# Kernel tuning notes

Hardware: AMD Instinct MI355X
Metric: run time of the kernel (lower is better)

## Reference

```python
import jax, jax.numpy as jnp
import numpy as np

SIGMA = 1.0   # noise std (unit-variance synthetic input)
P = 11        # patch size p1
K = 16        # number of similar patches k1
WIN = 65      # search window w (odd)
S = 3         # reference-patch stride
ALPHA = 0.5   # n2n alpha


def _unfold(x, ksize, stride):
    # (N,1,H,W) -> (N, ksize*ksize, Ho, Wo); kernel positions row-major (== torch F.unfold for C=1)
    return jax.lax.conv_general_dilated_patches(
        x, (ksize, ksize), (stride, stride), 'VALID',
        dimension_numbers=('NCHW', 'OIHW', 'NCHW'))


def block_matching(x, k, p, w, s):
    N, _, H, W = x.shape
    v = w // 2
    assert (H - p + 1) % s == 1 and (W - p + 1) % s == 1  # no edge-case branches needed
    Href = (H - p) // s + 1
    Wref = (W - p) // s + 1
    x_pad = jnp.pad(x, ((0, 0), (0, 0), (v, v), (v, v)))  # zero pad; invalid candidates masked below
    # |patch|^2 / p^2 at every position of the padded image (== F.avg_pool2d(x**2, p))
    sq = jax.lax.reduce_window(x_pad * x_pad, 0.0, jax.lax.add,
                               (1, 1, p, p), (1, 1, 1, 1), 'VALID') / (p * p)
    norms = _unfold(sq, 2 * v + 1, s)                                  # (N,(2v+1)^2,Href,Wref)
    norms = norms.reshape(N, 2 * v + 1, 2 * v + 1, Href, Wref).transpose(0, 3, 4, 1, 2)
    lw = _unfold(x_pad, 2 * v + p, s) / p                              # (N,(2v+p)^2,Href,Wref)
    lw = lw.reshape(N, 2 * v + p, 2 * v + p, Href, Wref).transpose(0, 3, 4, 1, 2)
    G = N * Href * Wref
    lw = lw.reshape(1, G, 2 * v + p, 2 * v + p)
    ref = lw[0, :, v:-v, v:-v][:, None]                                # (G,1,p,p) reference patches
    sp = jax.lax.conv_general_dilated(
        lw, ref, (1, 1), 'VALID',
        dimension_numbers=('NCHW', 'OIHW', 'NCHW'),
        feature_group_count=G)                                         # (1,G,2v+1,2v+1)
    dist = norms.reshape(1, G, 2 * v + 1, 2 * v + 1) - 2.0 * sp
    dist = dist.reshape(N, Href, Wref, 2 * v + 1, 2 * v + 1)
    # mask candidate patches that fall outside the original image (torch uses NaN padding + topk)
    offs = jnp.arange(-v, v + 1)
    hr = jnp.arange(Href) * s
    wr = jnp.arange(Wref) * s
    row_ok = (hr[:, None] + offs >= 0) & (hr[:, None] + offs <= H - p)  # (Href, 2v+1)
    col_ok = (wr[:, None] + offs >= 0) & (wr[:, None] + offs <= W - p)  # (Wref, 2v+1)
    valid = row_ok[:, None, :, None] & col_ok[None, :, None, :]
    dist = jnp.where(valid[None], dist, jnp.inf)
    dist = dist.at[..., v, v].set(-jnp.inf)                            # reference patch always kept
    dist = dist.reshape(N, Href, Wref, (2 * v + 1) ** 2)
    _, idx = jax.lax.top_k(-dist, k)                                   # k smallest distances
    ind_row = idx // (2 * v + 1) - v
    ind_col = idx % (2 * v + 1) - v
    ind = (ind_row + hr[None, :, None, None]) * (W - p + 1) + (ind_col + wr[None, None, :, None])
    return ind.reshape(N, -1)                                          # (N, Href*Wref*k)


def gather_groups(y, indices, k, p):
    N = y.shape[0]
    uf = _unfold(y, p, 1).reshape(N, p * p, -1)                        # (N, n, (H-p+1)(W-p+1))
    Yg = jnp.take_along_axis(uf, indices[:, None, :], axis=2)          # (N, n, L*k)
    L = indices.shape[1] // k
    return Yg.reshape(N, p * p, L, k).transpose(0, 2, 3, 1)            # (N, L, k, n)


def denoise1(Y, sigma):
    # method='n2n', constraints='affine'
    N, B, k, n = Y.shape
    D = n * sigma ** 2
    E = n * ALPHA ** 2 * sigma ** 2
    Ik = jnp.eye(k, dtype=Y.dtype)
    Q = Y @ jnp.swapaxes(Y, 2, 3) + E * Ik                             # (N,B,k,k), SPD
    Lc = jnp.linalg.cholesky(Q)
    Ikb = jnp.broadcast_to(Ik, Q.shape)
    Z = jax.scipy.linalg.solve_triangular(Lc, Ikb, lower=True)
    Qinv = jax.scipy.linalg.solve_triangular(jnp.swapaxes(Lc, 2, 3), Z, lower=False)
    Qinv1 = jnp.sum(Qinv, axis=3, keepdims=True)
    Qinv2 = jnp.sum(Qinv1, axis=2, keepdims=True)
    theta = Ik - (Qinv - (Qinv1 @ jnp.swapaxes(Qinv1, 2, 3)) / Qinv2) * (D + E)
    theta = jnp.swapaxes(theta, 2, 3)
    X_hat = theta @ Y
    weights = 1.0 / jnp.clip(jnp.sum(theta * theta, axis=3, keepdims=True), 1.0 / k, 1.0)
    return X_hat, weights


def _fold(x, H, W, p):
    # inverse of unfold: sum overlapping p x p patches back onto the image grid
    N, n, _ = x.shape
    Hp, Wp = H - p + 1, W - p + 1
    x = x.reshape(N, p, p, Hp, Wp)
    out = jnp.zeros((N, 1, H, W), x.dtype)
    for a in range(p):
        for b in range(p):
            out = out.at[:, 0, a:a + Hp, b:b + Wp].add(x[:, a, b])
    return out


def aggregate(X_hat, weights, indices, H, W, p):
    N, L, k, n = X_hat.shape
    X = (X_hat * weights).reshape(N, L * k, n).transpose(0, 2, 1)      # (N, n, L*k)
    Wt = jnp.broadcast_to(weights, (N, L, k, n)).reshape(N, L * k, n).transpose(0, 2, 1)
    Lfull = (H - p + 1) * (W - p + 1)
    def scat(vals, idx):
        return jnp.zeros((n, Lfull), vals.dtype).at[:, idx].add(vals)
    X_sum = jax.vmap(scat)(X, indices)
    W_sum = jax.vmap(scat)(Wt, indices)
    return _fold(X_sum, H, W, p) / _fold(W_sum, H, W, p)


def _forward(y):
    N, C, H, W = y.shape
    indices = block_matching(y, K, P, WIN, S)
    Yg = gather_groups(y, indices, K, P)
    X_hat, weights = denoise1(Yg, SIGMA)
    return aggregate(X_hat, weights, indices, H, W, P)


def setup_inputs():
    key = jax.random.key(0)
    y = jax.random.normal(key, (4, 1, 128, 128), dtype=jnp.float32)
    return {"y": y}


def reference(y):
    return _forward(y)
```

## Files before the change

### kernel.cpp

```cpp
#include <hip/hip_runtime.h>
#include <math.h>

#define HH 128
#define WW 128
#define NIMG 4
#define PP 11
#define KSIM 16
#define STRIDE_S 3
#define VRAD 32
#define WINW 65
#define NTASK (WINW*9)
#define HREF 40
#define WREF 40
#define NPOS 118
#define WROWS 75
#define WPITCH 84
#define NGROUP (NIMG*HREF*WREF)
#define EPS_E 30.25f
#define DE_C 151.25f
#define INFD 3.0e38f
#define RTASK (VRAD*9 + VRAD/8)

#define TDIM 4
#define NTIL (HREF/TDIM)
#define FOOT 84
#define FPITCH 85

__global__ __launch_bounds__(256, 4)
void bm_kernel(const float* __restrict__ y, int* __restrict__ inds)
{
    __shared__ float win[WROWS][WPITCH];
    __shared__ float swv[4];
    __shared__ int   swi[4];

    const int blk = blockIdx.x;
    const int n   = blk / (HREF*WREF);
    const int rem = blk % (HREF*WREF);
    const int hr  = (rem / WREF) * STRIDE_S;
    const int wr  = (rem % WREF) * STRIDE_S;
    const float* img = y + n * HH * WW;
    const int tid = threadIdx.x;

    for (int t = tid; t < WROWS * WPITCH; t += 256) {
        int r = t / WPITCH, c = t % WPITCH;
        int gr = hr - VRAD + r, gc = wr - VRAD + c;
        float v = 0.f;
        if (c < WROWS && gr >= 0 && gr < HH && gc >= 0 && gc < WW)
            v = img[gr * WW + gc];
        win[r][c] = v;
    }
    __syncthreads();

    float d[3][8];
#pragma unroll
    for (int s = 0; s < 3; s++)
#pragma unroll
        for (int c = 0; c < 8; c++) d[s][c] = INFD;

#pragma unroll
    for (int s = 0; s < 3; s++) {
        int task = tid + (s << 8);
        if (task < NTASK) {
            int drx = task / 9;
            int c0  = (task % 9) * 8;
            int rr  = hr + drx - VRAD;
            bool rowok = (rr >= 0 && rr <= HH - PP);
            if (rowok) {
                float dot[8];
                float colsq[18];
#pragma unroll
                for (int c = 0; c < 8; c++) dot[c] = 0.f;
#pragma unroll
                for (int j2 = 0; j2 < 18; j2++) colsq[j2] = 0.f;
                for (int a = 0; a < PP; a++) {
                    const float* wrow = &win[drx + a][c0];
                    const float* rrow = &win[VRAD + a][VRAD];
                    float wv[18];
#pragma unroll
                    for (int j2 = 0; j2 < 18; j2++) wv[j2] = wrow[j2];
#pragma unroll
                    for (int j2 = 0; j2 < 18; j2++) colsq[j2] += wv[j2] * wv[j2];
#pragma unroll
                    for (int b = 0; b < PP; b++) {
                        float rv = rrow[b];
#pragma unroll
                        for (int c = 0; c < 8; c++)
                            dot[c] += wv[b + c] * rv;
                    }
                }
#pragma unroll
                for (int j2 = 1; j2 < 18; j2++) colsq[j2] += colsq[j2 - 1];
#pragma unroll
                for (int c = 0; c < 8; c++) {
                    int dcx = c0 + c;
                    int cc  = wr + dcx - VRAD;
                    float norm = colsq[c + 10] - (c ? colsq[c - 1] : 0.f);
                    if (dcx < WINW && cc >= 0 && cc <= WW - PP)
                        d[s][c] = norm - 2.f * dot[c];
                }
            }
            if (task == RTASK) d[s][0] = -INFD;
        }
    }

    float lval = INFD; int lidx = 0;
#pragma unroll
    for (int s = 0; s < 3; s++)
#pragma unroll
        for (int c = 0; c < 8; c++)
            if (d[s][c] < lval) { lval = d[s][c]; lidx = (s << 3) | c; }

    for (int sel = 0; sel < KSIM; sel++) {
        float rv = lval;
        int   ri = ((tid + ((lidx >> 3) << 8)) << 3) | (lidx & 7);
#pragma unroll
        for (int off = 32; off > 0; off >>= 1) {
            float ov = __shfl_down(rv, off);
            int   oi = __shfl_down(ri, off);
            if (ov < rv) { rv = ov; ri = oi; }
        }
        if ((tid & 63) == 0) { swv[tid >> 6] = rv; swi[tid >> 6] = ri; }
        __syncthreads();
        float bval = swv[0]; int bidx = swi[0];
#pragma unroll
        for (int w2 = 1; w2 < 4; w2++)
            if (swv[w2] < bval) { bval = swv[w2]; bidx = swi[w2]; }
        if (tid == 0) {
            int task = bidx >> 3;
            int drx = task / 9, dcx = (task % 9) * 8 + (bidx & 7);
            int prr = hr + drx - VRAD, pcc = wr + dcx - VRAD;
            inds[blk * KSIM + sel] = prr * NPOS + pcc;
        }
        __syncthreads();
        int otid = (bidx >> 3) & 255;
        if (tid == otid) {
            int code = (((bidx >> 3) >> 8) << 3) | (bidx & 7);
            lval = INFD; lidx = 0;
#pragma unroll
            for (int s = 0; s < 3; s++)
#pragma unroll
                for (int c = 0; c < 8; c++) {
                    if (((s << 3) | c) == code) d[s][c] = INFD;
                    if (d[s][c] < lval) { lval = d[s][c]; lidx = (s << 3) | c; }
                }
        }
    }
}

__global__ __launch_bounds__(256, 2)
void dn_kernel(const float* __restrict__ y, const int* __restrict__ inds,
               float2* __restrict__ nd, int R)
{
    __shared__ float2 acc[FOOT][FPITCH];

    const int blk = blockIdx.x;
    const int n  = blk / (NTIL*NTIL);
    const int tr = blk % (NTIL*NTIL);
    const int ti = tr / NTIL, tj = tr % NTIL;
    const int tid = threadIdx.x;
    const int r0 = 3*(ti*TDIM) - VRAD;
    const int c0 = 3*(tj*TDIM) - VRAD;
    const float* img = y + n * HH * WW;

    {
        float* af = (float*)acc;
        for (int t = tid; t < FOOT*FPITCH*2; t += 256) af[t] = 0.f;
    }
    __syncthreads();

    const int wv2  = tid >> 6;
    const int lane = tid & 63;
    const int sg   = lane >> 4;
    const int r    = lane & 15;
    const int g    = n * (HREF*WREF) + (ti*TDIM + wv2) * WREF + (tj*TDIM + sg);

    const int idx  = inds[g * KSIM + r];
    const int prow = idx / NPOS, pcol = idx % NPOS;
    const float* pbase = img + prow * WW + pcol;

    float q[16];
#pragma unroll
    for (int m = 0; m < 16; m++) q[m] = (m == r) ? EPS_E : 0.f;
    for (int a = 0; a < PP; a++) {
        float yr[PP];
#pragma unroll
        for (int b = 0; b < PP; b++) yr[b] = pbase[a * WW + b];
#pragma unroll
        for (int b = 0; b < PP; b++) {
            float yj = yr[b];
#pragma unroll
            for (int m = 0; m < 16; m++) {
                float ym = __shfl(yj, m, 16);
                q[m] += yj * ym;
            }
        }
    }

#pragma unroll
    for (int c = 0; c < 16; c++) {
        float dc = __shfl(q[c], c, 16);
        float s  = sqrtf(dc);
        float inv = 1.f / s;
        q[c] = (r == c) ? s : q[c] * inv;
#pragma unroll
        for (int b = c + 1; b < 16; b++) {
            float lb = __shfl(q[c], b, 16);
            q[b] -= q[c] * lb;
        }
    }

    float z[16];
#pragma unroll
    for (int rr = 0; rr < 16; rr++) {
        float s = (rr == r) ? 1.f : 0.f;
        float diag = 0.f;
#pragma unroll
        for (int m = 0; m <= rr; m++) {
            float lrm = __shfl(q[m], rr, 16);
            if (m < rr) s -= lrm * z[m];
            else diag = lrm;
        }
        z[rr] = s / diag;
    }
    float x[16];
#pragma unroll
    for (int rr = 15; rr >= 0; rr--) {
        float s = z[rr];
        float diag = 0.f;
#pragma unroll
        for (int m = 15; m >= rr; m--) {
            float lmr = __shfl(q[rr], m, 16);
            if (m > rr) s -= lmr * x[m];
            else diag = lmr;
        }
        x[rr] = s / diag;
    }

    float s1 = 0.f;
#pragma unroll
    for (int b = 0; b < 16; b++) s1 += x[b];
    float s2 = s1;
#pragma unroll
    for (int mask = 1; mask < 16; mask <<= 1) s2 += __shfl_xor(s2, mask, 16);
    float th[16], tsq = 0.f;
#pragma unroll
    for (int b = 0; b < 16; b++) {
        float s1b = __shfl(s1, b, 16);
        float t = ((b == r) ? 1.f : 0.f) - (x[b] - s1 * s1b / s2) * DE_C;
        th[b] = t;
        tsq += t * t;
    }
    tsq = fminf(fmaxf(tsq, 1.f / (float)KSIM), 1.f);
    const float w = 1.f / tsq;

    const int arow = prow - r0, acol = pcol - c0;
    for (int a = 0; a < PP; a++) {
        float yr[PP];
#pragma unroll
        for (int b = 0; b < PP; b++) yr[b] = pbase[a * WW + b];
#pragma unroll
        for (int b = 0; b < PP; b++) {
            float yj = yr[b];
            float xh = 0.f;
#pragma unroll
            for (int m = 0; m < 16; m++) {
                float ym = __shfl(yj, m, 16);
                xh += th[m] * ym;
            }
            float2* cell = &acc[arow + a][acol + b];
            atomicAdd(&cell->x, w * xh);
            atomicAdd(&cell->y, w);
        }
    }
    __syncthreads();

    float2* ndI = nd + ((size_t)(blk & (R - 1)) * NIMG + n) * HH * WW;
    for (int t = tid; t < FOOT * FOOT; t += 256) {
        int rr = t / FOOT, cc = t % FOOT;
        float2 v = acc[rr][cc];
        if (v.y != 0.f) {
            int gr = r0 + rr, gc = c0 + cc;
            int px = gr * WW + gc;
#if defined(__has_builtin) && __has_builtin(__builtin_amdgcn_global_atomic_fadd_v2f32)
            typedef float v2f __attribute__((ext_vector_type(2)));
            __builtin_amdgcn_global_atomic_fadd_v2f32((v2f*)&ndI[px], (v2f){v.x, v.y});
#else
            atomicAdd(&ndI[px].x, v.x);
            atomicAdd(&ndI[px].y, v.y);
#endif
        }
    }
}

__global__ __launch_bounds__(256)
void fin_kernel(const float2* __restrict__ nd, float* __restrict__ out, int R)
{
    int t = blockIdx.x * 256 + threadIdx.x;
    if (t < NIMG * HH * WW) {
        float sn = 0.f, sd = 0.f;
        for (int r = 0; r < R; r++) {
            float2 v = nd[(size_t)r * NIMG * HH * WW + t];
            sn += v.x; sd += v.y;
        }
        out[t] = sn / sd;
    }
}

extern "C" void kernel_launch(void* const* d_in, const int* in_sizes, int n_in,
                              void* d_out, int out_size, void* d_ws, size_t ws_size,
                              hipStream_t stream)
{
    const float* y = (const float*)d_in[0];
    float* out = (float*)d_out;

    size_t indsBytes = (size_t)NGROUP * KSIM * sizeof(int);
    size_t perRep    = (size_t)NIMG * HH * WW * sizeof(float2);
    int R = 1;
    while (R < 4 && indsBytes + perRep * (size_t)(R * 2) <= ws_size) R <<= 1;

    float2* nd  = (float2*)d_ws;
    int*    inds = (int*)((char*)d_ws + perRep * (size_t)R);

    hipMemsetAsync(nd, 0, perRep * (size_t)R, stream);
    bm_kernel<<<NGROUP, 256, 0, stream>>>(y, inds);
    dn_kernel<<<NIMG * NTIL * NTIL, 256, 0, stream>>>(y, inds, nd, R);
    fin_kernel<<<(NIMG * HH * WW + 255) / 256, 256, 0, stream>>>(nd, out, R);
}
```

Measured before the change: 476.6 us.

## Rewrite denoise kernel with shared-memory tile and Gauss-Jordan inverse, vectorize BM loads

The denoise kernel now stages the image footprint in shared memory, computes the 16 Gram matrices cooperatively across 512 threads, and inverts them with a parallel Gauss-Jordan sweep in LDS. This replaces the per-lane shuffle-based Cholesky and triangular solves. The output projection is then done as a small matmul with shared atomics. The block-matching kernel switches to float4/float2 LDS loads and raises its occupancy hint. In exchange, Gauss-Jordan without pivoting needs more barriers and may be less numerically stable than Cholesky.

```diff
diff --git a/kernel.cpp b/kernel.cpp
--- a/kernel.cpp
+++ b/kernel.cpp
@@ -21,12 +21,11 @@
 #define INFD 3.0e38f
 #define RTASK (VRAD*9 + VRAD/8)
 
-#define TDIM 4
-#define NTIL (HREF/TDIM)
 #define FOOT 84
 #define FPITCH 85
-
-__global__ __launch_bounds__(256, 4)
+#define SPITCH 88
+
+__global__ __launch_bounds__(256, 5)
 void bm_kernel(const float* __restrict__ y, int* __restrict__ inds)
 {
     __shared__ float win[WROWS][WPITCH];
@@ -73,19 +72,25 @@
 #pragma unroll
                 for (int j2 = 0; j2 < 18; j2++) colsq[j2] = 0.f;
                 for (int a = 0; a < PP; a++) {
-                    const float* wrow = &win[drx + a][c0];
-                    const float* rrow = &win[VRAD + a][VRAD];
-                    float wv[18];
-#pragma unroll
-                    for (int j2 = 0; j2 < 18; j2++) wv[j2] = wrow[j2];
+                    const float4* w4 = reinterpret_cast<const float4*>(&win[drx + a][c0]);
+                    float4 A0 = w4[0], A1 = w4[1], A2 = w4[2], A3 = w4[3];
+                    float2 A4 = *reinterpret_cast<const float2*>(&win[drx + a][c0 + 16]);
+                    float wv[18] = {A0.x,A0.y,A0.z,A0.w, A1.x,A1.y,A1.z,A1.w,
+                                    A2.x,A2.y,A2.z,A2.w, A3.x,A3.y,A3.z,A3.w,
+                                    A4.x,A4.y};
+                    const float4* r4 = reinterpret_cast<const float4*>(&win[VRAD + a][VRAD]);
+                    float4 R0 = r4[0], R1 = r4[1];
+                    float2 R2 = *reinterpret_cast<const float2*>(&win[VRAD + a][VRAD + 8]);
+                    float  R3 = win[VRAD + a][VRAD + 10];
+                    float rv[11] = {R0.x,R0.y,R0.z,R0.w, R1.x,R1.y,R1.z,R1.w,
+                                    R2.x,R2.y, R3};
 #pragma unroll
                     for (int j2 = 0; j2 < 18; j2++) colsq[j2] += wv[j2] * wv[j2];
 #pragma unroll
                     for (int b = 0; b < PP; b++) {
-                        float rv = rrow[b];
 #pragma unroll
                         for (int c = 0; c < 8; c++)
-                            dot[c] += wv[b + c] * rv;
+                            dot[c] += wv[b + c] * rv[b];
                     }
                 }
 #pragma unroll
@@ -147,140 +152,176 @@
     }
 }
 
-__global__ __launch_bounds__(256, 2)
+__global__ __launch_bounds__(512, 1)
 void dn_kernel(const float* __restrict__ y, const int* __restrict__ inds,
                float2* __restrict__ nd, int R)
 {
+    __shared__ float  src[FOOT][SPITCH];
     __shared__ float2 acc[FOOT][FPITCH];
+    __shared__ float  Qm[16][16][17];
+    __shared__ float  s1[16][16];
+    __shared__ float  s2[16];
+    __shared__ float  wl[16][16];
+    __shared__ short  pr_[16][16], pc_[16][16];
 
     const int blk = blockIdx.x;
-    const int n  = blk / (NTIL*NTIL);
-    const int tr = blk % (NTIL*NTIL);
-    const int ti = tr / NTIL, tj = tr % NTIL;
+    const int n  = blk / 100;
+    const int tr = blk % 100;
+    const int ti = tr / 10, tj = tr % 10;
+    const int r0 = 12*ti - VRAD, c0 = 12*tj - VRAD;
     const int tid = threadIdx.x;
-    const int r0 = 3*(ti*TDIM) - VRAD;
-    const int c0 = 3*(tj*TDIM) - VRAD;
     const float* img = y + n * HH * WW;
 
+    if (tid < 256) {
+        int g = tid >> 4, m = tid & 15;
+        int gg = n*(HREF*WREF) + (ti*4 + (g >> 2))*WREF + (tj*4 + (g & 3));
+        int idx = inds[gg*KSIM + m];
+        pr_[g][m] = (short)(idx / NPOS);
+        pc_[g][m] = (short)(idx % NPOS);
+    }
+    for (int t = tid; t < FOOT*FOOT; t += 512) {
+        int rr = t / FOOT, cc = t % FOOT;
+        int gr = r0 + rr, gc = c0 + cc;
+        float v = 0.f;
+        if (gr >= 0 && gr < HH && gc >= 0 && gc < WW) v = img[gr*WW + gc];
+        src[rr][cc] = v;
+    }
+    for (int t = tid; t < FOOT*FPITCH; t += 512)
+        acc[t/FPITCH][t%FPITCH] = make_float2(0.f, 0.f);
+    __syncthreads();
+
+    for (int k = 0; k < 5; k++) {
+        int task = tid + k*512;
+        if (task < 16*136) {
+            int g = task / 136, e = task % 136;
+            int i = (int)((sqrtf(8.f*(float)e + 1.f) - 1.f) * 0.5f + 1e-4f);
+            int j = e - i*(i+1)/2;
+            int ari = pr_[g][i] - r0, aci = pc_[g][i] - c0;
+            int arj = pr_[g][j] - r0, acj = pc_[g][j] - c0;
+            float s = (i == j) ? EPS_E : 0.f;
+            for (int a = 0; a < PP; a++) {
+                const float* Ri = &src[ari + a][aci];
+                const float* Rj = &src[arj + a][acj];
+#pragma unroll
+                for (int b = 0; b < PP; b++) s += Ri[b] * Rj[b];
+            }
+            Qm[g][i][j] = s;
+            Qm[g][j][i] = s;
+        }
+    }
+    __syncthreads();
+
+    const int uu = tid >> 8, ii = (tid >> 4) & 15, jj = tid & 15;
+    for (int ks = 0; ks < 16; ks++) {
+        float fA[8], rk[8], pv[8], aij[8];
+#pragma unroll
+        for (int k = 0; k < 8; k++) {
+            int g = uu + 2*k;
+            fA[k]  = Qm[g][ii][ks];
+            rk[k]  = Qm[g][ks][jj];
+            pv[k]  = Qm[g][ks][ks];
+            aij[k] = Qm[g][ii][jj];
+        }
+        __syncthreads();
+#pragma unroll
+        for (int k = 0; k < 8; k++) {
+            int g = uu + 2*k;
+            float inv = 1.f / pv[k];
+            float nv;
+            if (ii == ks) nv = (jj == ks) ? inv : rk[k] * inv;
+            else          nv = (jj == ks) ? -fA[k] * inv : aij[k] - fA[k] * rk[k] * inv;
+            Qm[g][ii][jj] = nv;
+        }
+        __syncthreads();
+    }
+
+    if (tid < 256) {
+        int g = tid >> 4, a = tid & 15;
+        float s = 0.f;
+#pragma unroll
+        for (int b = 0; b < 16; b++) s += Qm[g][a][b];
+        s1[g][a] = s;
+    }
+    __syncthreads();
+    if (tid < 16) {
+        float s = 0.f;
+#pragma unroll
+        for (int a = 0; a < 16; a++) s += s1[tid][a];
+        s2[tid] = s;
+    }
+    __syncthreads();
+#pragma unroll
+    for (int k = 0; k < 8; k++) {
+        int g = uu + 2*k;
+        float t = ((ii == jj) ? 1.f : 0.f)
+                - (Qm[g][ii][jj] - s1[g][ii]*s1[g][jj]/s2[g]) * DE_C;
+        Qm[g][ii][jj] = t;
+    }
+    __syncthreads();
+    if (tid < 256) {
+        int g = tid >> 4, r = tid & 15;
+        float s = 0.f;
+#pragma unroll
+        for (int m2 = 0; m2 < 16; m2++) { float t = Qm[g][m2][r]; s += t*t; }
+        s = fminf(fmaxf(s, 1.f/16.f), 1.f);
+        wl[g][r] = 1.f / s;
+    }
+    __syncthreads();
+
     {
-        float* af = (float*)acc;
-        for (int t = tid; t < FOOT*FPITCH*2; t += 256) af[t] = 0.f;
-    }
-    __syncthreads();
-
-    const int wv2  = tid >> 6;
-    const int lane = tid & 63;
-    const int sg   = lane >> 4;
-    const int r    = lane & 15;
-    const int g    = n * (HREF*WREF) + (ti*TDIM + wv2) * WREF + (tj*TDIM + sg);
-
-    const int idx  = inds[g * KSIM + r];
-    const int prow = idx / NPOS, pcol = idx % NPOS;
-    const float* pbase = img + prow * WW + pcol;
-
-    float q[16];
-#pragma unroll
-    for (int m = 0; m < 16; m++) q[m] = (m == r) ? EPS_E : 0.f;
-    for (int a = 0; a < PP; a++) {
-        float yr[PP];
-#pragma unroll
-        for (int b = 0; b < PP; b++) yr[b] = pbase[a * WW + b];
-#pragma unroll
-        for (int b = 0; b < PP; b++) {
-            float yj = yr[b];
-#pragma unroll
-            for (int m = 0; m < 16; m++) {
-                float ym = __shfl(yj, m, 16);
-                q[m] += yj * ym;
+        const int g6 = tid >> 5, q6 = tid & 31;
+        const int pxb = q6 * 4;
+        int drp[4], dcp[4]; bool okp[4];
+#pragma unroll
+        for (int p = 0; p < 4; p++) {
+            int px = pxb + p;
+            okp[p] = (px < 121);
+            int pxc = okp[p] ? px : 0;
+            drp[p] = pxc / 11; dcp[p] = pxc % 11;
+        }
+        float xh[16][4];
+#pragma unroll
+        for (int r = 0; r < 16; r++)
+#pragma unroll
+            for (int p = 0; p < 4; p++) xh[r][p] = 0.f;
+#pragma unroll
+        for (int m2 = 0; m2 < 16; m2++) {
+            int ar = pr_[g6][m2] - r0, ac = pc_[g6][m2] - c0;
+            float tv[16];
+#pragma unroll
+            for (int r = 0; r < 16; r++) tv[r] = Qm[g6][m2][r];
+            float yv[4];
+#pragma unroll
+            for (int p = 0; p < 4; p++) yv[p] = src[ar + drp[p]][ac + dcp[p]];
+#pragma unroll
+            for (int r = 0; r < 16; r++)
+#pragma unroll
+                for (int p = 0; p < 4; p++) xh[r][p] += tv[r] * yv[p];
+        }
+#pragma unroll
+        for (int r = 0; r < 16; r++) {
+            int ar = pr_[g6][r] - r0, ac = pc_[g6][r] - c0;
+            float wv2 = wl[g6][r];
+#pragma unroll
+            for (int p = 0; p < 4; p++) {
+                if (okp[p]) {
+                    float* cell = (float*)&acc[ar + drp[p]][ac + dcp[p]];
+                    __hip_atomic_fetch_add(cell,     wv2 * xh[r][p],
+                        __ATOMIC_RELAXED, __HIP_MEMORY_SCOPE_WORKGROUP);
+                    __hip_atomic_fetch_add(cell + 1, wv2,
+                        __ATOMIC_RELAXED, __HIP_MEMORY_SCOPE_WORKGROUP);
+                }
             }
         }
     }
-
-#pragma unroll
-    for (int c = 0; c < 16; c++) {
-        float dc = __shfl(q[c], c, 16);
-        float s  = sqrtf(dc);
-        float inv = 1.f / s;
-        q[c] = (r == c) ? s : q[c] * inv;
-#pragma unroll
-        for (int b = c + 1; b < 16; b++) {
-            float lb = __shfl(q[c], b, 16);
-            q[b] -= q[c] * lb;
-        }
-    }
-
-    float z[16];
-#pragma unroll
-    for (int rr = 0; rr < 16; rr++) {
-        float s = (rr == r) ? 1.f : 0.f;
-        float diag = 0.f;
-#pragma unroll
-        for (int m = 0; m <= rr; m++) {
-            float lrm = __shfl(q[m], rr, 16);
-            if (m < rr) s -= lrm * z[m];
-            else diag = lrm;
-        }
-        z[rr] = s / diag;
-    }
-    float x[16];
-#pragma unroll
-    for (int rr = 15; rr >= 0; rr--) {
-        float s = z[rr];
-        float diag = 0.f;
-#pragma unroll
-        for (int m = 15; m >= rr; m--) {
-            float lmr = __shfl(q[rr], m, 16);
-            if (m > rr) s -= lmr * x[m];
-            else diag = lmr;
-        }
-        x[rr] = s / diag;
-    }
-
-    float s1 = 0.f;
-#pragma unroll
-    for (int b = 0; b < 16; b++) s1 += x[b];
-    float s2 = s1;
-#pragma unroll
-    for (int mask = 1; mask < 16; mask <<= 1) s2 += __shfl_xor(s2, mask, 16);
-    float th[16], tsq = 0.f;
-#pragma unroll
-    for (int b = 0; b < 16; b++) {
-        float s1b = __shfl(s1, b, 16);
-        float t = ((b == r) ? 1.f : 0.f) - (x[b] - s1 * s1b / s2) * DE_C;
-        th[b] = t;
-        tsq += t * t;
-    }
-    tsq = fminf(fmaxf(tsq, 1.f / (float)KSIM), 1.f);
-    const float w = 1.f / tsq;
-
-    const int arow = prow - r0, acol = pcol - c0;
-    for (int a = 0; a < PP; a++) {
-        float yr[PP];
-#pragma unroll
-        for (int b = 0; b < PP; b++) yr[b] = pbase[a * WW + b];
-#pragma unroll
-        for (int b = 0; b < PP; b++) {
-            float yj = yr[b];
-            float xh = 0.f;
-#pragma unroll
-            for (int m = 0; m < 16; m++) {
-                float ym = __shfl(yj, m, 16);
-                xh += th[m] * ym;
-            }
-            float2* cell = &acc[arow + a][acol + b];
-            atomicAdd(&cell->x, w * xh);
-            atomicAdd(&cell->y, w);
-        }
-    }
     __syncthreads();
 
     float2* ndI = nd + ((size_t)(blk & (R - 1)) * NIMG + n) * HH * WW;
-    for (int t = tid; t < FOOT * FOOT; t += 256) {
+    for (int t = tid; t < FOOT * FOOT; t += 512) {
         int rr = t / FOOT, cc = t % FOOT;
         float2 v = acc[rr][cc];
         if (v.y != 0.f) {
-            int gr = r0 + rr, gc = c0 + cc;
-            int px = gr * WW + gc;
+            int px = (r0 + rr) * WW + (c0 + cc);
 #if defined(__has_builtin) && __has_builtin(__builtin_amdgcn_global_atomic_fadd_v2f32)
             typedef float v2f __attribute__((ext_vector_type(2)));
             __builtin_amdgcn_global_atomic_fadd_v2f32((v2f*)&ndI[px], (v2f){v.x, v.y});
@@ -323,6 +364,6 @@
 
     hipMemsetAsync(nd, 0, perRep * (size_t)R, stream);
     bm_kernel<<<NGROUP, 256, 0, stream>>>(y, inds);
-    dn_kernel<<<NIMG * NTIL * NTIL, 256, 0, stream>>>(y, inds, nd, R);
+    dn_kernel<<<NIMG * 100, 512, 0, stream>>>(y, inds, nd, R);
     fin_kernel<<<(NIMG * HH * WW + 255) / 256, 256, 0, stream>>>(nd, out, R);
 }
```

Result: slower. 492.3 us (+3.3%).
